# Kernel tuning notes

Hardware: AMD Instinct MI355X
Metric: run time of the kernel (lower is better)

Reference implementation:

```python
import jax, jax.numpy as jnp
import numpy as np

N_NODES = 200000
N_EDGES = 6400000
F_IN = 128
F_HID = 64


def setup_inputs() -> dict:
    key = jax.random.key(0)
    k1, k2, k3, k4, k5, k6, k7 = jax.random.split(key, 7)
    x = jax.random.normal(k1, (N_NODES, F_IN), dtype=jnp.float32)
    edge_index = jax.random.randint(k2, (2, N_EDGES), 0, N_NODES, dtype=jnp.int64)
    edge_weights = jax.random.uniform(k3, (N_EDGES,), dtype=jnp.float32)
    # GCNConv params: PyG Linear stores weight as [out, in]; glorot-ish init
    s1 = 1.0 / np.sqrt(F_IN)
    s2 = 1.0 / np.sqrt(F_HID)
    W1 = jax.random.uniform(k4, (F_HID, F_IN), dtype=jnp.float32, minval=-s1, maxval=s1)
    b1 = jax.random.uniform(k5, (F_HID,), dtype=jnp.float32, minval=-s1, maxval=s1)
    W2 = jax.random.uniform(k6, (F_IN, F_HID), dtype=jnp.float32, minval=-s2, maxval=s2)
    b2 = jax.random.uniform(k7, (F_IN,), dtype=jnp.float32, minval=-s2, maxval=s2)
    return {"x": x, "edge_index": edge_index, "edge_weights": edge_weights,
            "W1": W1, "b1": b1, "W2": W2, "b2": b2}


def reference(x, edge_index, edge_weights, W1, b1, W2, b2):
    N = x.shape[0]
    row, col = edge_index[0], edge_index[1]  # source -> target
    # symmetric normalization (add_self_loops=False): deg over targets
    deg = jax.ops.segment_sum(edge_weights, col, num_segments=N)
    deg_inv_sqrt = jnp.where(deg > 0, jax.lax.rsqrt(deg), 0.0)
    norm = deg_inv_sqrt[row] * edge_weights * deg_inv_sqrt[col]  # [E]

    def gcn(h, W, b):
        h = h @ W.T  # dense linear transform [N, out]
        msg = norm[:, None] * h[row]  # gather + weight, [E, out]
        agg = jax.ops.segment_sum(msg, col, num_segments=N)  # scatter-add
        return agg + b

    h = jax.nn.relu(gcn(x, W1, b1))
    return jax.nn.relu(gcn(h, W2, b2))
```

## Files before the change

kernel.cpp:

```cpp
#include <hip/hip_runtime.h>
#include <stdint.h>

#define FIN 128
#define FHID 64
#define CHUNK 2048
#define FIX_SCALE 65536.0f
#define FIX_INV   (1.0f / 65536.0f)
#define AGG_SC    262144.0f
#define AGG_INV   (1.0f / 262144.0f)

__device__ __forceinline__ float bf2f(unsigned short u) {
    union { unsigned int i; float f; } v; v.i = ((unsigned int)u) << 16; return v.f;
}
__device__ __forceinline__ unsigned short f2bf(float f) {
    union { float f; unsigned int i; } v; v.f = f;
    unsigned int u = v.i;
    u += 0x7FFFu + ((u >> 16) & 1u);
    return (unsigned short)(u >> 16);
}

__global__ void k_detect(const uint32_t* __restrict__ ei, int* __restrict__ flag) {
    if (blockIdx.x == 0 && threadIdx.x == 0) {
        uint32_t o = 0;
        #pragma unroll
        for (int i = 1; i < 16; i += 2) o |= ei[i];
        *flag = (o == 0) ? 1 : 0;
    }
}

__device__ __forceinline__ int edge_at(const void* ei, long long idx, int is64) {
    if (is64) return (int)((const long long*)ei)[idx];
    return ((const int*)ei)[idx];
}

__global__ __launch_bounds__(256) void k_deg(const void* __restrict__ ei, const float* __restrict__ w,
                                             unsigned int* __restrict__ packed,
                                             unsigned char* __restrict__ rank,
                                             const int* __restrict__ flag, int E) {
    int e = blockIdx.x * 256 + threadIdx.x;
    if (e >= E) return;
    int is64 = *flag;
    int c = edge_at(ei, (long long)E + e, is64);
    unsigned int inc = (1u << 24) | __float2uint_rn(w[e] * FIX_SCALE);
    unsigned int old = atomicAdd(&packed[c], inc);
    rank[e] = (unsigned char)(old >> 24);
}

__global__ __launch_bounds__(256) void k_dis(const unsigned int* __restrict__ packed,
                                             float* __restrict__ dis, int N) {
    int i = blockIdx.x * 256 + threadIdx.x;
    if (i < N) {
        float d = (float)(packed[i] & 0xFFFFFFu) * FIX_INV;
        dis[i] = (d > 0.f) ? rsqrtf(d) : 0.f;
    }
}

__global__ __launch_bounds__(256) void k_scan_part(const unsigned int* __restrict__ packed,
                                                   int* __restrict__ partial, int N) {
    __shared__ int sdata[256];
    int b = blockIdx.x, t = threadIdx.x;
    int base = b * CHUNK;
    int sum = 0;
    #pragma unroll
    for (int q = 0; q < CHUNK / 256; ++q) {
        int idx = base + q * 256 + t;
        if (idx < N) sum += (int)(packed[idx] >> 24);
    }
    sdata[t] = sum; __syncthreads();
    for (int off = 128; off > 0; off >>= 1) {
        if (t < off) sdata[t] += sdata[t + off];
        __syncthreads();
    }
    if (t == 0) partial[b] = sdata[0];
}

__global__ void k_scan_top(int* partial, int nparts, int* row_start, int N) {
    if (blockIdx.x == 0 && threadIdx.x == 0) {
        int run = 0;
        for (int i = 0; i < nparts; ++i) { int v = partial[i]; partial[i] = run; run += v; }
        row_start[N] = run;
    }
}

__global__ __launch_bounds__(256) void k_scan_chunk(const unsigned int* __restrict__ packed,
                                                    const int* __restrict__ partial,
                                                    int* __restrict__ row_start, int N) {
    __shared__ int tsum[256];
    __shared__ int toff[256];
    int b = blockIdx.x, t = threadIdx.x;
    int base = b * CHUNK + t * 8;
    int v[8]; int s = 0;
    #pragma unroll
    for (int q = 0; q < 8; ++q) {
        int idx = base + q;
        v[q] = (idx < N) ? (int)(packed[idx] >> 24) : 0;
        s += v[q];
    }
    tsum[t] = s; __syncthreads();
    if (t == 0) {
        int run = partial[b];
        for (int i = 0; i < 256; ++i) { int x = tsum[i]; toff[i] = run; run += x; }
    }
    __syncthreads();
    int ex = toff[t];
    #pragma unroll
    for (int q = 0; q < 8; ++q) {
        int idx = base + q;
        if (idx < N) row_start[idx] = ex;
        ex += v[q];
    }
}

__global__ __launch_bounds__(256) void k_fill(const void* __restrict__ ei, const float* __restrict__ w,
                                              const float* __restrict__ dis,
                                              const int* __restrict__ row_start,
                                              const unsigned char* __restrict__ rank,
                                              int2* __restrict__ csr,
                                              const int* __restrict__ flag, int E) {
    int e = blockIdx.x * 256 + threadIdx.x;
    if (e >= E) return;
    int is64 = *flag;
    int r = edge_at(ei, e, is64);
    int c = edge_at(ei, (long long)E + e, is64);
    float nm = dis[r] * w[e] * dis[c];
    int pos = row_start[c] + (int)rank[e];
    csr[pos] = make_int2(r, __float_as_int(nm));
}

__global__ __launch_bounds__(256) void k_w2t(const float* __restrict__ W2, float* __restrict__ W2t) {
    int i = blockIdx.x * 256 + threadIdx.x;
    if (i < FIN * FHID) {
        int j = i >> 6, k = i & 63;
        W2t[k * FIN + j] = W2[i];
    }
}

__global__ __launch_bounds__(256, 4) void k_gemm1(const float* __restrict__ x, const float* __restrict__ W1,
                                                  unsigned short* __restrict__ h1lin, int N) {
    __shared__ float Wt[FIN * 65];
    __shared__ float xt[32 * FIN];
    int t = threadIdx.x;
    for (int i = t; i < FHID * FIN; i += 256) {
        int j = i >> 7, k = i & 127;
        Wt[k * 65 + j] = W1[i];
    }
    int r0 = blockIdx.x * 32;
    const float4* xg = (const float4*)(x + (size_t)r0 * FIN);
    float4* xt4 = (float4*)xt;
    #pragma unroll
    for (int q = 0; q < 4; ++q) {
        int i = t + q * 256;
        if (r0 + (i >> 5) < N) xt4[i] = xg[i];
    }
    __syncthreads();
    int j = t & 63, rg = t >> 6;
    float acc[8];
    #pragma unroll
    for (int r = 0; r < 8; ++r) acc[r] = 0.f;
    for (int kk = 0; kk < FIN; kk += 4) {
        float w0 = Wt[(kk + 0) * 65 + j];
        float w1 = Wt[(kk + 1) * 65 + j];
        float w2 = Wt[(kk + 2) * 65 + j];
        float w3 = Wt[(kk + 3) * 65 + j];
        #pragma unroll
        for (int r = 0; r < 8; ++r) {
            float4 xv = xt4[(rg * 8 + r) * 32 + (kk >> 2)];
            acc[r] += xv.x * w0 + xv.y * w1 + xv.z * w2 + xv.w * w3;
        }
    }
    #pragma unroll
    for (int r = 0; r < 8; ++r) {
        int row = r0 + rg * 8 + r;
        if (row < N) h1lin[(size_t)row * FHID + j] = f2bf(acc[r]);
    }
}


__global__ __launch_bounds__(256) void k_agg1(const int2* __restrict__ csr, const int* __restrict__ row_start,
                                              const unsigned int* __restrict__ tab32,
                                              const float* __restrict__ b1,
                                              unsigned int* __restrict__ h1_32, int N) {
    int wid = threadIdx.x >> 6, lane = threadIdx.x & 63;
    int nodeA = blockIdx.x * 8 + wid * 2;
    if (nodeA >= N) return;
    int nodeB = nodeA + 1;
    bool hasB = nodeB < N;
    int half = lane >> 5, lpos = lane & 31;
    int baseA = row_start[nodeA], eA = row_start[nodeA + 1];
    int baseB = hasB ? eA : 0, eB = hasB ? row_start[nodeB + 1] : 0;
    int aAx0 = 0, aAy0 = 0, aAx1 = 0, aAy1 = 0;
    int aBx0 = 0, aBy0 = 0, aBx1 = 0, aBy1 = 0;
    while (baseA < eA || baseB < eB) {
        int mA = eA - baseA; mA = mA < 0 ? 0 : (mA > 64 ? 64 : mA);
        int mB = eB - baseB; mB = mB < 0 ? 0 : (mB > 64 ? 64 : mB);
        int2 entA = (lane < mA) ? csr[baseA + lane] : make_int2(0, 0);
        int2 entB = (lane < mB) ? csr[baseB + lane] : make_int2(0, 0);
        int mMax = mA > mB ? mA : mB;
        int i = 0;
        for (; i + 4 <= mMax; i += 4) {
            if (i < mA) {
                int s0 = __shfl(entA.x, i + half);     float n0 = __shfl(__int_as_float(entA.y), i + half);
                int s1 = __shfl(entA.x, i + 2 + half); float n1 = __shfl(__int_as_float(entA.y), i + 2 + half);
                unsigned v0 = tab32[(size_t)((unsigned)s0 << 5) + lpos];
                unsigned v1 = tab32[(size_t)((unsigned)s1 << 5) + lpos];
                float f0 = n0 * AGG_SC, f1 = n1 * AGG_SC;
                aAx0 += __float2int_rz(f0 * bf2f((unsigned short)v0));
                aAy0 += __float2int_rz(f0 * bf2f((unsigned short)(v0 >> 16)));
                aAx1 += __float2int_rz(f1 * bf2f((unsigned short)v1));
                aAy1 += __float2int_rz(f1 * bf2f((unsigned short)(v1 >> 16)));
            }
            if (i < mB) {
                int s0 = __shfl(entB.x, i + half);     float n0 = __shfl(__int_as_float(entB.y), i + half);
                int s1 = __shfl(entB.x, i + 2 + half); float n1 = __shfl(__int_as_float(entB.y), i + 2 + half);
                unsigned v0 = tab32[(size_t)((unsigned)s0 << 5) + lpos];
                unsigned v1 = tab32[(size_t)((unsigned)s1 << 5) + lpos];
                float f0 = n0 * AGG_SC, f1 = n1 * AGG_SC;
                aBx0 += __float2int_rz(f0 * bf2f((unsigned short)v0));
                aBy0 += __float2int_rz(f0 * bf2f((unsigned short)(v0 >> 16)));
                aBx1 += __float2int_rz(f1 * bf2f((unsigned short)v1));
                aBy1 += __float2int_rz(f1 * bf2f((unsigned short)(v1 >> 16)));
            }
        }
        for (; i < mMax; ++i) {
            if (i < mA) {
                int s0 = __shfl(entA.x, i); float n0 = __shfl(__int_as_float(entA.y), i);
                if (half) n0 = 0.f;
                unsigned v0 = tab32[(size_t)((unsigned)s0 << 5) + lpos];
                float f0 = n0 * AGG_SC;
                aAx0 += __float2int_rz(f0 * bf2f((unsigned short)v0));
                aAy0 += __float2int_rz(f0 * bf2f((unsigned short)(v0 >> 16)));
            }
            if (i < mB) {
                int s0 = __shfl(entB.x, i); float n0 = __shfl(__int_as_float(entB.y), i);
                if (half) n0 = 0.f;
                unsigned v0 = tab32[(size_t)((unsigned)s0 << 5) + lpos];
                float f0 = n0 * AGG_SC;
                aBx0 += __float2int_rz(f0 * bf2f((unsigned short)v0));
                aBy0 += __float2int_rz(f0 * bf2f((unsigned short)(v0 >> 16)));
            }
        }
        baseA += 64; baseB += 64;
    }
    int axA = aAx0 + aAx1, ayA = aAy0 + aAy1;
    axA += __shfl_xor(axA, 32); ayA += __shfl_xor(ayA, 32);
    int axB = aBx0 + aBx1, ayB = aBy0 + aBy1;
    axB += __shfl_xor(axB, 32); ayB += __shfl_xor(ayB, 32);
    if (lane < 32) {
        float2 bp = ((const float2*)b1)[lane];
        unsigned rA = (unsigned)f2bf(fmaxf((float)axA * AGG_INV + bp.x, 0.f))
                    | ((unsigned)f2bf(fmaxf((float)ayA * AGG_INV + bp.y, 0.f)) << 16);
        h1_32[(size_t)nodeA * 32 + lane] = rA;
        if (hasB) {
            unsigned rB = (unsigned)f2bf(fmaxf((float)axB * AGG_INV + bp.x, 0.f))
                        | ((unsigned)f2bf(fmaxf((float)ayB * AGG_INV + bp.y, 0.f)) << 16);
            h1_32[(size_t)nodeB * 32 + lane] = rB;
        }
    }
}

__global__ __launch_bounds__(256) void k_agg2f(const int2* __restrict__ csr, const int* __restrict__ row_start,
                                               const unsigned int* __restrict__ tab32,
                                               const float* __restrict__ W2t,
                                               const float* __restrict__ b2, float* __restrict__ out, int N) {
    int wid = threadIdx.x >> 6, lane = threadIdx.x & 63;
    int nodeA = blockIdx.x * 8 + wid * 2;
    if (nodeA >= N) return;
    int nodeB = nodeA + 1;
    bool hasB = nodeB < N;
    int half = lane >> 5, lpos = lane & 31;
    int baseA = row_start[nodeA], eA = row_start[nodeA + 1];
    int baseB = hasB ? eA : 0, eB = hasB ? row_start[nodeB + 1] : 0;
    float aAx0 = 0.f, aAy0 = 0.f, aAx1 = 0.f, aAy1 = 0.f;
    float aBx0 = 0.f, aBy0 = 0.f, aBx1 = 0.f, aBy1 = 0.f;
    while (baseA < eA || baseB < eB) {
        int mA = eA - baseA; mA = mA < 0 ? 0 : (mA > 64 ? 64 : mA);
        int mB = eB - baseB; mB = mB < 0 ? 0 : (mB > 64 ? 64 : mB);
        int2 entA = (lane < mA) ? csr[baseA + lane] : make_int2(0, 0);
        int2 entB = (lane < mB) ? csr[baseB + lane] : make_int2(0, 0);
        int mMax = mA > mB ? mA : mB;
        int i = 0;
        for (; i + 4 <= mMax; i += 4) {
            if (i < mA) {
                int s0 = __shfl(entA.x, i + half);     float n0 = __shfl(__int_as_float(entA.y), i + half);
                int s1 = __shfl(entA.x, i + 2 + half); float n1 = __shfl(__int_as_float(entA.y), i + 2 + half);
                unsigned v0 = tab32[(size_t)((unsigned)s0 << 5) + lpos];
                unsigned v1 = tab32[(size_t)((unsigned)s1 << 5) + lpos];
                aAx0 += n0 * bf2f((unsigned short)v0);
                aAy0 += n0 * bf2f((unsigned short)(v0 >> 16));
                aAx1 += n1 * bf2f((unsigned short)v1);
                aAy1 += n1 * bf2f((unsigned short)(v1 >> 16));
            }
            if (i < mB) {
                int s0 = __shfl(entB.x, i + half);     float n0 = __shfl(__int_as_float(entB.y), i + half);
                int s1 = __shfl(entB.x, i + 2 + half); float n1 = __shfl(__int_as_float(entB.y), i + 2 + half);
                unsigned v0 = tab32[(size_t)((unsigned)s0 << 5) + lpos];
                unsigned v1 = tab32[(size_t)((unsigned)s1 << 5) + lpos];
                aBx0 += n0 * bf2f((unsigned short)v0);
                aBy0 += n0 * bf2f((unsigned short)(v0 >> 16));
                aBx1 += n1 * bf2f((unsigned short)v1);
                aBy1 += n1 * bf2f((unsigned short)(v1 >> 16));
            }
        }
        for (; i < mMax; ++i) {
            if (i < mA) {
                int s0 = __shfl(entA.x, i); float n0 = __shfl(__int_as_float(entA.y), i);
                if (half) n0 = 0.f;
                unsigned v0 = tab32[(size_t)((unsigned)s0 << 5) + lpos];
                aAx0 += n0 * bf2f((unsigned short)v0);
                aAy0 += n0 * bf2f((unsigned short)(v0 >> 16));
            }
            if (i < mB) {
                int s0 = __shfl(entB.x, i); float n0 = __shfl(__int_as_float(entB.y), i);
                if (half) n0 = 0.f;
                unsigned v0 = tab32[(size_t)((unsigned)s0 << 5) + lpos];
                aBx0 += n0 * bf2f((unsigned short)v0);
                aBy0 += n0 * bf2f((unsigned short)(v0 >> 16));
            }
        }
        baseA += 64; baseB += 64;
    }
    float axA = aAx0 + aAx1, ayA = aAy0 + aAy1;
    axA += __shfl_xor(axA, 32); ayA += __shfl_xor(ayA, 32);
    float axB = aBx0 + aBx1, ayB = aBy0 + aBy1;
    axB += __shfl_xor(axB, 32); ayB += __shfl_xor(ayB, 32);
    {
        float o0 = b2[lane], o1 = b2[lane + 64];
        #pragma unroll 4
        for (int p = 0; p < 32; ++p) {
            float ae = __shfl(axA, p);
            float ao = __shfl(ayA, p);
            o0 += ae * W2t[(2 * p) * FIN + lane]      + ao * W2t[(2 * p + 1) * FIN + lane];
            o1 += ae * W2t[(2 * p) * FIN + 64 + lane] + ao * W2t[(2 * p + 1) * FIN + 64 + lane];
        }
        out[(size_t)nodeA * FIN + lane] = fmaxf(o0, 0.f);
        out[(size_t)nodeA * FIN + 64 + lane] = fmaxf(o1, 0.f);
    }
    if (hasB) {
        float o0 = b2[lane], o1 = b2[lane + 64];
        #pragma unroll 4
        for (int p = 0; p < 32; ++p) {
            float ae = __shfl(axB, p);
            float ao = __shfl(ayB, p);
            o0 += ae * W2t[(2 * p) * FIN + lane]      + ao * W2t[(2 * p + 1) * FIN + lane];
            o1 += ae * W2t[(2 * p) * FIN + 64 + lane] + ao * W2t[(2 * p + 1) * FIN + 64 + lane];
        }
        out[(size_t)nodeB * FIN + lane] = fmaxf(o0, 0.f);
        out[(size_t)nodeB * FIN + 64 + lane] = fmaxf(o1, 0.f);
    }
}

extern "C" void kernel_launch(void* const* d_in, const int* in_sizes, int n_in,
                              void* d_out, int out_size, void* d_ws, size_t ws_size,
                              hipStream_t stream) {
    const float* x  = (const float*)d_in[0];
    const void*  ei = d_in[1];
    const float* w  = (const float*)d_in[2];
    const float* W1 = (const float*)d_in[3];
    const float* b1 = (const float*)d_in[4];
    const float* W2 = (const float*)d_in[5];
    const float* b2 = (const float*)d_in[6];
    float* out = (float*)d_out;
    int N = in_sizes[0] / FIN;
    int E = in_sizes[2];

    char* ws = (char*)d_ws;
    size_t off = 0;
    auto alloc = [&](size_t b) { size_t o = off; off = (off + b + 255) & ~255ULL; return o; };
    int*   flag      = (int*)(ws + alloc(4));
    unsigned int* packed = (unsigned int*)(ws + alloc((size_t)N * 4));
    float* dis       = (float*)(ws + alloc((size_t)N * 4));
    int*   row_start = (int*)(ws + alloc((size_t)(N + 1) * 4));
    int*   partial   = (int*)(ws + alloc(4096));
    float* W2t       = (float*)(ws + alloc((size_t)FIN * FHID * 4));
    int2*  csr       = (int2*)(ws + alloc((size_t)E * 8));
    unsigned int* h1_32    = (unsigned int*)(ws + alloc((size_t)N * FHID * 2));
    unsigned int* h1lin32  = (unsigned int*)(ws + alloc((size_t)N * FHID * 2));
    unsigned char* rank = (unsigned char*)h1lin32;

    hipMemsetAsync(packed, 0, (size_t)N * 4, stream);

    k_detect<<<1, 64, 0, stream>>>((const uint32_t*)ei, flag);

    int eb = (E + 255) / 256;
    k_deg<<<eb, 256, 0, stream>>>(ei, w, packed, rank, flag, E);
    k_dis<<<(N + 255) / 256, 256, 0, stream>>>(packed, dis, N);

    int nparts = (N + CHUNK - 1) / CHUNK;
    k_scan_part<<<nparts, 256, 0, stream>>>(packed, partial, N);
    k_scan_top<<<1, 64, 0, stream>>>(partial, nparts, row_start, N);
    k_scan_chunk<<<nparts, 256, 0, stream>>>(packed, partial, row_start, N);

    k_fill<<<eb, 256, 0, stream>>>(ei, w, dis, row_start, rank, csr, flag, E);
    k_w2t<<<(FIN * FHID + 255) / 256, 256, 0, stream>>>(W2, W2t);

    k_gemm1<<<(N + 31) / 32, 256, 0, stream>>>(x, W1, (unsigned short*)h1lin32, N);
    k_agg1<<<(N + 7) / 8, 256, 0, stream>>>(csr, row_start, h1lin32, b1, h1_32, N);
    k_agg2f<<<(N + 7) / 8, 256, 0, stream>>>(csr, row_start, h1_32, W2t, b2, out, N);
}
```

Measured before the change: 994.0 us.

## Split layer-2 aggregation from its GEMM and use fixed-point agg for both layers

Replaces the fused float aggregate-then-matvec layer-2 kernel with a templated fixed-point aggregation shared by both layers, which writes bf16 aggregates. A separate shared-memory tiled GEMM kernel then applies W2, bias and ReLU. The aim is to take the per-node shuffle-based matvec, with its repeated global W2t reads, out of the latency-bound gather kernel and make the gather lighter. In exchange it adds an extra N×64 bf16 intermediate round trip and one more launch, and rounds the layer-2 aggregate to bf16 before the GEMM.

After: 984.5 us. About the same (-1.0%).

```diff
diff --git a/kernel.cpp b/kernel.cpp
--- a/kernel.cpp
+++ b/kernel.cpp
@@ -127,14 +127,6 @@
     csr[pos] = make_int2(r, __float_as_int(nm));
 }
 
-__global__ __launch_bounds__(256) void k_w2t(const float* __restrict__ W2, float* __restrict__ W2t) {
-    int i = blockIdx.x * 256 + threadIdx.x;
-    if (i < FIN * FHID) {
-        int j = i >> 6, k = i & 63;
-        W2t[k * FIN + j] = W2[i];
-    }
-}
-
 __global__ __launch_bounds__(256, 4) void k_gemm1(const float* __restrict__ x, const float* __restrict__ W1,
                                                   unsigned short* __restrict__ h1lin, int N) {
     __shared__ float Wt[FIN * 65];
@@ -175,11 +167,11 @@
     }
 }
 
-
-__global__ __launch_bounds__(256) void k_agg1(const int2* __restrict__ csr, const int* __restrict__ row_start,
-                                              const unsigned int* __restrict__ tab32,
-                                              const float* __restrict__ b1,
-                                              unsigned int* __restrict__ h1_32, int N) {
+template <int OUT_MODE>
+__device__ __forceinline__ void agg_fx_dual(const int2* __restrict__ csr, const int* __restrict__ row_start,
+                                            const unsigned int* __restrict__ tab32,
+                                            const float* __restrict__ b1,
+                                            unsigned int* __restrict__ out32, int N) {
     int wid = threadIdx.x >> 6, lane = threadIdx.x & 63;
     int nodeA = blockIdx.x * 8 + wid * 2;
     if (nodeA >= N) return;
@@ -246,106 +238,72 @@
     int axB = aBx0 + aBx1, ayB = aBy0 + aBy1;
     axB += __shfl_xor(axB, 32); ayB += __shfl_xor(ayB, 32);
     if (lane < 32) {
-        float2 bp = ((const float2*)b1)[lane];
-        unsigned rA = (unsigned)f2bf(fmaxf((float)axA * AGG_INV + bp.x, 0.f))
-                    | ((unsigned)f2bf(fmaxf((float)ayA * AGG_INV + bp.y, 0.f)) << 16);
-        h1_32[(size_t)nodeA * 32 + lane] = rA;
-        if (hasB) {
-            unsigned rB = (unsigned)f2bf(fmaxf((float)axB * AGG_INV + bp.x, 0.f))
-                        | ((unsigned)f2bf(fmaxf((float)ayB * AGG_INV + bp.y, 0.f)) << 16);
-            h1_32[(size_t)nodeB * 32 + lane] = rB;
-        }
-    }
-}
-
-__global__ __launch_bounds__(256) void k_agg2f(const int2* __restrict__ csr, const int* __restrict__ row_start,
-                                               const unsigned int* __restrict__ tab32,
-                                               const float* __restrict__ W2t,
-                                               const float* __restrict__ b2, float* __restrict__ out, int N) {
-    int wid = threadIdx.x >> 6, lane = threadIdx.x & 63;
-    int nodeA = blockIdx.x * 8 + wid * 2;
-    if (nodeA >= N) return;
-    int nodeB = nodeA + 1;
-    bool hasB = nodeB < N;
-    int half = lane >> 5, lpos = lane & 31;
-    int baseA = row_start[nodeA], eA = row_start[nodeA + 1];
-    int baseB = hasB ? eA : 0, eB = hasB ? row_start[nodeB + 1] : 0;
-    float aAx0 = 0.f, aAy0 = 0.f, aAx1 = 0.f, aAy1 = 0.f;
-    float aBx0 = 0.f, aBy0 = 0.f, aBx1 = 0.f, aBy1 = 0.f;
-    while (baseA < eA || baseB < eB) {
-        int mA = eA - baseA; mA = mA < 0 ? 0 : (mA > 64 ? 64 : mA);
-        int mB = eB - baseB; mB = mB < 0 ? 0 : (mB > 64 ? 64 : mB);
-        int2 entA = (lane < mA) ? csr[baseA + lane] : make_int2(0, 0);
-        int2 entB = (lane < mB) ? csr[baseB + lane] : make_int2(0, 0);
-        int mMax = mA > mB ? mA : mB;
-        int i = 0;
-        for (; i + 4 <= mMax; i += 4) {
-            if (i < mA) {
-                int s0 = __shfl(entA.x, i + half);     float n0 = __shfl(__int_as_float(entA.y), i + half);
-                int s1 = __shfl(entA.x, i + 2 + half); float n1 = __shfl(__int_as_float(entA.y), i + 2 + half);
-                unsigned v0 = tab32[(size_t)((unsigned)s0 << 5) + lpos];
-                unsigned v1 = tab32[(size_t)((unsigned)s1 << 5) + lpos];
-                aAx0 += n0 * bf2f((unsigned short)v0);
-                aAy0 += n0 * bf2f((unsigned short)(v0 >> 16));
-                aAx1 += n1 * bf2f((unsigned short)v1);
-                aAy1 += n1 * bf2f((unsigned short)(v1 >> 16));
-            }
-            if (i < mB) {
-                int s0 = __shfl(entB.x, i + half);     float n0 = __shfl(__int_as_float(entB.y), i + half);
-                int s1 = __shfl(entB.x, i + 2 + half); float n1 = __shfl(__int_as_float(entB.y), i + 2 + half);
-                unsigned v0 = tab32[(size_t)((unsigned)s0 << 5) + lpos];
-                unsigned v1 = tab32[(size_t)((unsigned)s1 << 5) + lpos];
-                aBx0 += n0 * bf2f((unsigned short)v0);
-                aBy0 += n0 * bf2f((unsigned short)(v0 >> 16));
-                aBx1 += n1 * bf2f((unsigned short)v1);
-                aBy1 += n1 * bf2f((unsigned short)(v1 >> 16));
-            }
-        }
-        for (; i < mMax; ++i) {
-            if (i < mA) {
-                int s0 = __shfl(entA.x, i); float n0 = __shfl(__int_as_float(entA.y), i);
-                if (half) n0 = 0.f;
-                unsigned v0 = tab32[(size_t)((unsigned)s0 << 5) + lpos];
-                aAx0 += n0 * bf2f((unsigned short)v0);
-                aAy0 += n0 * bf2f((unsigned short)(v0 >> 16));
-            }
-            if (i < mB) {
-                int s0 = __shfl(entB.x, i); float n0 = __shfl(__int_as_float(entB.y), i);
-                if (half) n0 = 0.f;
-                unsigned v0 = tab32[(size_t)((unsigned)s0 << 5) + lpos];
-                aBx0 += n0 * bf2f((unsigned short)v0);
-                aBy0 += n0 * bf2f((unsigned short)(v0 >> 16));
-            }
-        }
-        baseA += 64; baseB += 64;
-    }
-    float axA = aAx0 + aAx1, ayA = aAy0 + aAy1;
-    axA += __shfl_xor(axA, 32); ayA += __shfl_xor(ayA, 32);
-    float axB = aBx0 + aBx1, ayB = aBy0 + aBy1;
-    axB += __shfl_xor(axB, 32); ayB += __shfl_xor(ayB, 32);
-    {
-        float o0 = b2[lane], o1 = b2[lane + 64];
-        #pragma unroll 4
-        for (int p = 0; p < 32; ++p) {
-            float ae = __shfl(axA, p);
-            float ao = __shfl(ayA, p);
-            o0 += ae * W2t[(2 * p) * FIN + lane]      + ao * W2t[(2 * p + 1) * FIN + lane];
-            o1 += ae * W2t[(2 * p) * FIN + 64 + lane] + ao * W2t[(2 * p + 1) * FIN + 64 + lane];
-        }
-        out[(size_t)nodeA * FIN + lane] = fmaxf(o0, 0.f);
-        out[(size_t)nodeA * FIN + 64 + lane] = fmaxf(o1, 0.f);
-    }
-    if (hasB) {
-        float o0 = b2[lane], o1 = b2[lane + 64];
-        #pragma unroll 4
-        for (int p = 0; p < 32; ++p) {
-            float ae = __shfl(axB, p);
-            float ao = __shfl(ayB, p);
-            o0 += ae * W2t[(2 * p) * FIN + lane]      + ao * W2t[(2 * p + 1) * FIN + lane];
-            o1 += ae * W2t[(2 * p) * FIN + 64 + lane] + ao * W2t[(2 * p + 1) * FIN + 64 + lane];
-        }
-        out[(size_t)nodeB * FIN + lane] = fmaxf(o0, 0.f);
-        out[(size_t)nodeB * FIN + 64 + lane] = fmaxf(o1, 0.f);
+        float fxA = (float)axA * AGG_INV, fyA = (float)ayA * AGG_INV;
+        float fxB = (float)axB * AGG_INV, fyB = (float)ayB * AGG_INV;
+        if (OUT_MODE == 0) {
+            float2 bp = ((const float2*)b1)[lane];
+            fxA = fmaxf(fxA + bp.x, 0.f); fyA = fmaxf(fyA + bp.y, 0.f);
+            fxB = fmaxf(fxB + bp.x, 0.f); fyB = fmaxf(fyB + bp.y, 0.f);
+        }
+        out32[(size_t)nodeA * 32 + lane] = (unsigned)f2bf(fxA) | ((unsigned)f2bf(fyA) << 16);
+        if (hasB)
+            out32[(size_t)nodeB * 32 + lane] = (unsigned)f2bf(fxB) | ((unsigned)f2bf(fyB) << 16);
+    }
+}
+
+__global__ __launch_bounds__(256) void k_agg1(const int2* __restrict__ csr, const int* __restrict__ row_start,
+                                              const unsigned int* __restrict__ h1lin32,
+                                              const float* __restrict__ b1,
+                                              unsigned int* __restrict__ h1_32, int N) {
+    agg_fx_dual<0>(csr, row_start, h1lin32, b1, h1_32, N);
+}
+
+__global__ __launch_bounds__(256) void k_agg2(const int2* __restrict__ csr, const int* __restrict__ row_start,
+                                              const unsigned int* __restrict__ h1_32,
+                                              unsigned int* __restrict__ aggv32, int N) {
+    agg_fx_dual<1>(csr, row_start, h1_32, (const float*)nullptr, aggv32, N);
+}
+
+#define G2_ROWS 16
+__global__ __launch_bounds__(256, 4) void k_gemm2(const unsigned int* __restrict__ aggv32,
+                                                  const float* __restrict__ W2,
+                                                  const float* __restrict__ b2,
+                                                  float* __restrict__ out, int N) {
+    __shared__ float Wt[FHID * 129];
+    __shared__ unsigned int at[G2_ROWS * 33];
+    int t = threadIdx.x;
+    for (int i = t; i < FIN * FHID; i += 256) {
+        int j = i >> 6, k = i & 63;
+        Wt[k * 129 + j] = W2[i];
+    }
+    int r0 = blockIdx.x * G2_ROWS;
+    for (int i = t; i < G2_ROWS * 32; i += 256) {
+        int r = i >> 5, c = i & 31;
+        at[r * 33 + c] = (r0 + r < N) ? aggv32[(size_t)(r0 + r) * 32 + c] : 0u;
+    }
+    __syncthreads();
+    int j = t & 127, rg = t >> 7;
+    float acc[8];
+    #pragma unroll
+    for (int r = 0; r < 8; ++r) acc[r] = 0.f;
+    for (int c = 0; c < 32; c += 2) {
+        float w0 = Wt[(2 * c + 0) * 129 + j];
+        float w1 = Wt[(2 * c + 1) * 129 + j];
+        float w2 = Wt[(2 * c + 2) * 129 + j];
+        float w3 = Wt[(2 * c + 3) * 129 + j];
+        #pragma unroll
+        for (int r = 0; r < 8; ++r) {
+            unsigned a01 = at[(rg * 8 + r) * 33 + c];
+            unsigned a23 = at[(rg * 8 + r) * 33 + c + 1];
+            acc[r] += bf2f((unsigned short)a01) * w0 + bf2f((unsigned short)(a01 >> 16)) * w1
+                    + bf2f((unsigned short)a23) * w2 + bf2f((unsigned short)(a23 >> 16)) * w3;
+        }
+    }
+    float bj = b2[j];
+    #pragma unroll
+    for (int r = 0; r < 8; ++r) {
+        int row = r0 + rg * 8 + r;
+        if (row < N) out[(size_t)row * FIN + j] = fmaxf(acc[r] + bj, 0.f);
     }
 }
 
@@ -371,9 +329,9 @@
     float* dis       = (float*)(ws + alloc((size_t)N * 4));
     int*   row_start = (int*)(ws + alloc((size_t)(N + 1) * 4));
     int*   partial   = (int*)(ws + alloc(4096));
-    float* W2t       = (float*)(ws + alloc((size_t)FIN * FHID * 4));
     int2*  csr       = (int2*)(ws + alloc((size_t)E * 8));
     unsigned int* h1_32    = (unsigned int*)(ws + alloc((size_t)N * FHID * 2));
+    unsigned int* aggv32   = (unsigned int*)(ws + alloc((size_t)N * FHID * 2));
     unsigned int* h1lin32  = (unsigned int*)(ws + alloc((size_t)N * FHID * 2));
     unsigned char* rank = (unsigned char*)h1lin32;
 
@@ -391,9 +349,9 @@
     k_scan_chunk<<<nparts, 256, 0, stream>>>(packed, partial, row_start, N);
 
     k_fill<<<eb, 256, 0, stream>>>(ei, w, dis, row_start, rank, csr, flag, E);
-    k_w2t<<<(FIN * FHID + 255) / 256, 256, 0, stream>>>(W2, W2t);
 
     k_gemm1<<<(N + 31) / 32, 256, 0, stream>>>(x, W1, (unsigned short*)h1lin32, N);
     k_agg1<<<(N + 7) / 8, 256, 0, stream>>>(csr, row_start, h1lin32, b1, h1_32, N);
-    k_agg2f<<<(N + 7) / 8, 256, 0, stream>>>(csr, row_start, h1_32, W2t, b2, out, N);
-}
+    k_agg2<<<(N + 7) / 8, 256, 0, stream>>>(csr, row_start, h1_32, aggv32, N);
+    k_gemm2<<<(N + G2_ROWS - 1) / G2_ROWS, 256, 0, stream>>>(aggv32, W2, b2, out, N);
+}
```
